# Performance work log

Measured on AMD Instinct MI355X. Metric: run time of the kernel, lower is better.

The kernel has to match this reference:

```python
import jax, jax.numpy as jnp
import numpy as np

N = 50000      # nodes
E = 800000     # edges (avg degree 16)
D = 64         # emb_dim
L = 5          # num_layer
BN_EPS = 1e-5


def setup_inputs() -> dict:
    key = jax.random.key(0)
    ks = jax.random.split(key, 10)
    x = jax.random.randint(ks[0], (N,), 0, 1)                      # indices into 1-row embedding
    edge_index = jax.random.randint(ks[1], (2, E), 0, N)
    edge_attr = jax.random.normal(ks[2], (E, 7), dtype=jnp.float32)
    s = lambda k, shape: (jax.random.normal(k, shape, dtype=jnp.float32) * 0.05)
    node_emb = s(ks[3], (1, D))
    # per-layer GINConv params, stacked on a leading layer axis for lax.scan
    We = s(ks[4], (L, 7, D));   be = jnp.zeros((L, D), jnp.float32)      # edge_encoder
    eps = jnp.zeros((L,), jnp.float32)                                   # GIN eps
    W1 = s(ks[5], (L, D, 2 * D)); b1 = jnp.zeros((L, 2 * D), jnp.float32)  # mlp linear1
    g1 = jnp.ones((L, 2 * D), jnp.float32); bb1 = jnp.zeros((L, 2 * D), jnp.float32)  # mlp BN
    W2 = s(ks[6], (L, 2 * D, D)); b2 = jnp.zeros((L, D), jnp.float32)    # mlp linear2
    g2 = jnp.ones((L, D), jnp.float32); bb2 = jnp.zeros((L, D), jnp.float32)  # outer BN
    return dict(x=x, edge_index=edge_index, edge_attr=edge_attr, node_emb=node_emb,
                We=We, be=be, eps=eps, W1=W1, b1=b1, g1=g1, bb1=bb1,
                W2=W2, b2=b2, g2=g2, bb2=bb2)


def _bn(a, g, b):
    # BatchNorm1d in training mode: batch statistics over node axis, biased var
    m = a.mean(axis=0)
    v = jnp.var(a, axis=0)
    return (a - m) * jax.lax.rsqrt(v + BN_EPS) * g + b


def reference(x, edge_index, edge_attr, node_emb, We, be, eps,
              W1, b1, g1, bb1, W2, b2, g2, bb2):
    src, dst = edge_index[0], edge_index[1]
    h = node_emb[x]                                    # [N, D]
    relu_flags = jnp.arange(L) < (L - 1)               # ReLU on all but last layer

    def step(h, p):
        We_, be_, eps_, W1_, b1_, g1_, bb1_, W2_, b2_, g2_, bb2_, flag = p
        ee = edge_attr @ We_ + be_                     # [E, D] edge embeddings
        msg = jax.nn.relu(h[src] + ee)                 # gather + elementwise
        agg = jax.ops.segment_sum(msg, dst, num_segments=N)  # scatter-add
        z = (1.0 + eps_) * h + agg                     # GIN combine
        a = jax.nn.relu(_bn(z @ W1_ + b1_, g1_, bb1_)) # mlp: lin -> BN -> ReLU
        hb = _bn(a @ W2_ + b2_, g2_, bb2_)             # lin -> outer BN
        h_new = jnp.where(flag, jax.nn.relu(hb), hb)   # dropout omitted (eval)
        return h_new, None

    h, _ = jax.lax.scan(step, h, (We, be, eps, W1, b1, g1, bb1, W2, b2, g2, bb2, relu_flags))
    return h                                           # JK='last'
```

## Files before the change

### kernel.cpp

```cpp
#include <hip/hip_runtime.h>
#include <hip/hip_fp16.h>

#define NN 50000
#define EE 800000
#define NB 782
#define NBKT 196
#define BCAP 5120

typedef _Float16 f16x8 __attribute__((ext_vector_type(8)));
typedef _Float16 f16x4 __attribute__((ext_vector_type(4)));
typedef _Float16 f16x2 __attribute__((ext_vector_type(2)));
typedef float f32x4 __attribute__((ext_vector_type(4)));

__device__ __forceinline__ unsigned h2u(__half2 h) {
    union { __half2 h; unsigned u; } c; c.h = h; return c.u;
}
__device__ __forceinline__ f16x2 u2h(unsigned u) {
    union { unsigned u; f16x2 h; } c; c.u = u; return c.h;
}

__global__ __launch_bounds__(256) void bin_kernel(
    const int* __restrict__ ei, const float* __restrict__ ea,
    int* __restrict__ bktcur, int4* __restrict__ srec,
    unsigned short* __restrict__ sdst)
{
    __shared__ int cnt[NBKT], base[NBKT];
    const int t = threadIdx.x;
    if (t < NBKT) cnt[t] = 0;
    __syncthreads();
    const int e0 = blockIdx.x << 10;
    int bkk[4], rk[4], loc[4];
#pragma unroll
    for (int j = 0; j < 4; ++j) {
        const int e = e0 + (j << 8) + t;
        if (e < EE) {
            const int d = ei[EE + e];
            bkk[j] = d >> 8;
            loc[j] = d & 255;
            rk[j] = atomicAdd(&cnt[bkk[j]], 1);
        } else bkk[j] = -1;
    }
    __syncthreads();
    if (t < NBKT) base[t] = cnt[t] ? atomicAdd(&bktcur[t], cnt[t]) : 0;
    __syncthreads();
#pragma unroll
    for (int j = 0; j < 4; ++j) {
        if (bkk[j] < 0) continue;
        const int slot = base[bkk[j]] + rk[j];
        if (slot >= BCAP) continue;
        const int pos = bkk[j] * BCAP + slot;
        const int e = e0 + (j << 8) + t;
        const int src = ei[e];
        const float* a = ea + e * 7;
        const unsigned h0 = __half_as_ushort(__float2half(a[0]));
        const unsigned h1 = __half_as_ushort(__float2half(a[1]));
        const unsigned h2 = __half_as_ushort(__float2half(a[2]));
        const unsigned h3 = __half_as_ushort(__float2half(a[3]));
        const unsigned h4 = __half_as_ushort(__float2half(a[4]));
        const unsigned h5 = __half_as_ushort(__float2half(a[5]));
        const unsigned h6 = __half_as_ushort(__float2half(a[6]));
        srec[pos] = make_int4((int)(h0 | (h1 << 16)), (int)(h2 | (h3 << 16)),
                              (int)(h4 | (h5 << 16)), (int)(h6 | ((unsigned)src << 16)));
        sdst[pos] = (unsigned short)loc[j];
    }
}

__global__ __launch_bounds__(256) void bcount2_kernel(
    const int* __restrict__ bktcur, const unsigned short* __restrict__ sdst,
    int* __restrict__ deg)
{
    __shared__ int nc[256];
    const int b = blockIdx.x, t = threadIdx.x;
    nc[t] = 0;
    __syncthreads();
    const int nEdge = bktcur[b];
    const int sbase = b * BCAP;
    for (int i = t; i < nEdge; i += 256) atomicAdd(&nc[(int)sdst[sbase + i]], 1);
    __syncthreads();
    const int node = (b << 8) + t;
    if (node < NN) deg[node] = nc[t];
}

__global__ __launch_bounds__(256) void scanA_kernel(const int* __restrict__ deg,
                                                    int* __restrict__ bsum) {
    __shared__ int sm[256];
    const int t = threadIdx.x;
    const int i = (blockIdx.x << 8) + t;
    sm[t] = (i < NN) ? ((deg[i] + 7) & ~7) : 0;
    __syncthreads();
    for (int o = 128; o > 0; o >>= 1) {
        if (t < o) sm[t] += sm[t + o];
        __syncthreads();
    }
    if (t == 0) bsum[blockIdx.x] = sm[0];
}

__global__ __launch_bounds__(256) void scanB_kernel(int* __restrict__ bsum) {
    __shared__ int sm[256];
    const int t = threadIdx.x;
    const int v = (t < 196) ? bsum[t] : 0;
    sm[t] = v;
    __syncthreads();
    for (int o = 1; o < 256; o <<= 1) {
        const int u = (t >= o) ? sm[t - o] : 0;
        __syncthreads();
        sm[t] += u;
        __syncthreads();
    }
    bsum[t] = sm[t] - v;
}

__global__ __launch_bounds__(256) void scanC_kernel(const int* __restrict__ deg,
                                                    const int* __restrict__ bsum,
                                                    int* __restrict__ off,
                                                    int* __restrict__ cur) {
    __shared__ int sm[256];
    const int t = threadIdx.x;
    const int i = (blockIdx.x << 8) + t;
    const int v = (i < NN) ? ((deg[i] + 7) & ~7) : 0;
    sm[t] = v;
    __syncthreads();
    for (int o = 1; o < 256; o <<= 1) {
        const int u = (t >= o) ? sm[t - o] : 0;
        __syncthreads();
        sm[t] += u;
        __syncthreads();
    }
    const int excl = bsum[blockIdx.x] + sm[t] - v;
    if (i < NN) { off[i] = excl; cur[i] = excl; }
    else if (i == NN) off[NN] = excl;
}

__global__ __launch_bounds__(256) void place2_kernel(
    const int* __restrict__ bktcur, const int* __restrict__ off,
    const int4* __restrict__ srec, const unsigned short* __restrict__ sdst,
    int4* __restrict__ pea)
{
    __shared__ int curs[256];
    const int b = blockIdx.x, t = threadIdx.x;
    const int node = (b << 8) + t;
    curs[t] = (node < NN) ? off[node] : 0;
    __syncthreads();
    const int nEdge = bktcur[b];
    const int sbase = b * BCAP;
    for (int i = t; i < nEdge; i += 256) {
        const int ln = (int)sdst[sbase + i];
        const int p = atomicAdd(&curs[ln], 1);
        pea[p] = srec[sbase + i];
    }
    __syncthreads();
    if (node < NN) {
        const int end = off[node + 1];
        for (int p = curs[t]; p < end; ++p)
            pea[p] = make_int4(0, 0, 0, (int)(((unsigned)NN) << 16));
    }
}

__global__ __launch_bounds__(256) void bnstats_kernel(
    const float* __restrict__ part, const int nb, const int half,
    const float* __restrict__ g, const float* __restrict__ bb,
    float* __restrict__ scsh)
{
    __shared__ float ss[256], qq[256];
    const int c = blockIdx.x, t = threadIdx.x;
    const int stride = half << 1;
    float s = 0.f, q = 0.f;
    for (int b = t; b < nb; b += 256) {
        s += part[b * stride + c];
        q += part[b * stride + half + c];
    }
    ss[t] = s; qq[t] = q;
    __syncthreads();
    for (int o = 128; o > 0; o >>= 1) {
        if (t < o) { ss[t] += ss[t + o]; qq[t] += qq[t + o]; }
        __syncthreads();
    }
    if (t == 0) {
        const float m = ss[0] * (1.0f / NN);
        const float v = fmaxf(qq[0] * (1.0f / NN) - m * m, 0.0f);
        const float sc = g[c] * rsqrtf(v + 1e-5f);
        scsh[c] = sc;
        scsh[half + c] = bb[c] - m * sc;
    }
}

__global__ __launch_bounds__(256) void wprep_kernel(
    const float* __restrict__ W1, const float* __restrict__ W2,
    const float* __restrict__ We, const float* __restrict__ be,
    _Float16* __restrict__ W1s, _Float16* __restrict__ W2s,
    unsigned* __restrict__ Wepk, unsigned* __restrict__ be2)
{
    const int i = (blockIdx.x << 8) + threadIdx.x;
    if (i < 40960) {
        const int l = i >> 13, j = i & 8191, k = j >> 7, n = j & 127;
        W1s[(l << 13) + ((((k >> 3) << 7) + n) << 3) + (k & 7)] = (_Float16)W1[i];
    } else if (i < 81920) {
        const int i2 = i - 40960;
        const int l = i2 >> 13, j = i2 & 8191, k = j >> 6, n = j & 63;
        W2s[(l << 13) + ((((k >> 3) << 6) + n) << 3) + (k & 7)] = (_Float16)W2[i2];
    } else if (i < 83040) {
        const int i3 = i - 81920;
        const int l = i3 / 224;
        const int r = i3 - l * 224;
        const int k = r >> 5, s = r & 31;
        const float* W = We + l * 448 + (k << 6) + (s << 1);
        Wepk[i3] = h2u(__floats2half2_rn(W[0], W[1]));
    } else if (i < 83200) {
        const int i4 = i - 83040;
        const int l = i4 >> 5, s = i4 & 31;
        const float* B = be + (l << 6) + (s << 1);
        be2[i4] = h2u(__floats2half2_rn(B[0], B[1]));
    }
}

__global__ __launch_bounds__(256) void hprep_kernel(
    const float* __restrict__ y2, const float* __restrict__ scsh2,
    __half* __restrict__ h16)
{
    const int i4 = (blockIdx.x << 8) + threadIdx.x;
    const float4 v = ((const float4*)y2)[i4];
    const int d0 = (i4 << 2) & 63;
    const float a = fmaxf(fmaf(v.x, scsh2[d0 + 0], scsh2[64 + d0 + 0]), 0.f);
    const float b = fmaxf(fmaf(v.y, scsh2[d0 + 1], scsh2[64 + d0 + 1]), 0.f);
    const float c = fmaxf(fmaf(v.z, scsh2[d0 + 2], scsh2[64 + d0 + 2]), 0.f);
    const float d = fmaxf(fmaf(v.w, scsh2[d0 + 3], scsh2[64 + d0 + 3]), 0.f);
    *(int2*)(h16 + (i4 << 2)) =
        make_int2((int)h2u(__floats2half2_rn(a, b)),
                  (int)h2u(__floats2half2_rn(c, d)));
}

__global__ __launch_bounds__(256) void hprep0_kernel(
    const int* __restrict__ x, const float* __restrict__ nemb,
    __half* __restrict__ h16, unsigned* __restrict__ z32)
{
    const int i4 = (blockIdx.x << 8) + threadIdx.x;
    if (blockIdx.x == 0 && threadIdx.x < 32)
        ((unsigned*)h16)[(NN << 5) + threadIdx.x] = 0xFBFFFBFFu;
    if (i4 < 1536) z32[1600000 + i4] = 0u;
    const int n = i4 >> 4;
    const float4 v = ((const float4*)nemb)[(x[n] << 4) + (i4 & 15)];
    *(int2*)(h16 + (i4 << 2)) =
        make_int2((int)h2u(__floats2half2_rn(v.x, v.y)),
                  (int)h2u(__floats2half2_rn(v.z, v.w)));
}

__global__ __launch_bounds__(256) void gather_kernel(
    const int* __restrict__ off, const int4* __restrict__ pea,
    const unsigned* __restrict__ h32,
    const unsigned* __restrict__ Wepk, const unsigned* __restrict__ be2,
    const float* __restrict__ epsp,
    unsigned* __restrict__ z32)
{
    const int t = threadIdx.x;
    const int lane = t & 63;
    const int s = lane & 31;
    const int n = (blockIdx.x << 3) + ((t >> 6) << 1) + (lane >> 5);

    const f16x2 w0 = u2h(Wepk[s]),       w1 = u2h(Wepk[32 + s]),
                w2 = u2h(Wepk[64 + s]),  w3 = u2h(Wepk[96 + s]),
                w4 = u2h(Wepk[128 + s]), w5 = u2h(Wepk[160 + s]),
                w6 = u2h(Wepk[192 + s]);
    const f16x2 beh = u2h(be2[s]);

    const int e0 = off[n], e1 = off[n + 1];

    f16x2 acc2 = (f16x2){(_Float16)0.f, (_Float16)0.f};
    for (int e = e0; e < e1; e += 8) {
        int4 pk[8];
#pragma unroll
        for (int j = 0; j < 8; ++j) pk[j] = pea[e + j];
        unsigned hv[8];
#pragma unroll
        for (int j = 0; j < 8; ++j) {
            const int src = (int)(((unsigned)pk[j].w) >> 16);
            hv[j] = h32[(src << 5) + s];
        }
#pragma unroll
        for (int j = 0; j < 8; ++j) {
            const f16x2 a01 = u2h((unsigned)pk[j].x);
            const f16x2 a23 = u2h((unsigned)pk[j].y);
            const f16x2 a45 = u2h((unsigned)pk[j].z);
            const f16x2 a6x = u2h((unsigned)pk[j].w);
            f16x2 ee = beh;
            ee += (f16x2){a01[0], a01[0]} * w0;
            ee += (f16x2){a01[1], a01[1]} * w1;
            ee += (f16x2){a23[0], a23[0]} * w2;
            ee += (f16x2){a23[1], a23[1]} * w3;
            ee += (f16x2){a45[0], a45[0]} * w4;
            ee += (f16x2){a45[1], a45[1]} * w5;
            ee += (f16x2){a6x[0], a6x[0]} * w6;
            f16x2 m2 = u2h(hv[j]) + ee;
            const _Float16 zz = (_Float16)0.f;
            m2 = (f16x2){ m2[0] > zz ? m2[0] : zz, m2[1] > zz ? m2[1] : zz };
            acc2 += m2;
        }
    }
    const f16x2 hn2 = u2h(h32[(n << 5) + s]);
    const float e1f = 1.0f + epsp[0];
    const float zLo = fmaf(e1f, (float)hn2[0], (float)acc2[0]);
    const float zHi = fmaf(e1f, (float)hn2[1], (float)acc2[1]);
    z32[(n << 5) + s] = h2u(__floats2half2_rn(zLo, zHi));
}

__global__ __launch_bounds__(256) void mm1_kernel(
    const _Float16* __restrict__ z16, const _Float16* __restrict__ W1s,
    const float* __restrict__ b1p, _Float16* __restrict__ y1h,
    float* __restrict__ part1)
{
    __shared__ float smS[4][128], smQ[4][128];
    const int t = threadIdx.x;
    const int wv = t >> 6, lane = t & 63;
    const int q = lane >> 4, ln = lane & 15;
    const int r0 = blockIdx.x << 6;

    const int rowm = r0 + (wv << 4) + ln;
    const f16x8 af0 = *(const f16x8*)(z16 + rowm * 64 + (q << 3));
    const f16x8 af1 = *(const f16x8*)(z16 + rowm * 64 + 32 + (q << 3));

    f32x4 acc[8];
#pragma unroll
    for (int n0 = 0; n0 < 8; ++n0) acc[n0] = (f32x4){0.f, 0.f, 0.f, 0.f};
#pragma unroll
    for (int n0 = 0; n0 < 8; ++n0) {
        const f16x8 bf0 = *(const f16x8*)(W1s + (((q << 7) + (n0 << 4) + ln) << 3));
        const f16x8 bf1 = *(const f16x8*)(W1s + ((((4 + q) << 7) + (n0 << 4) + ln) << 3));
        acc[n0] = __builtin_amdgcn_mfma_f32_16x16x32_f16(af0, bf0, acc[n0], 0, 0, 0);
        acc[n0] = __builtin_amdgcn_mfma_f32_16x16x32_f16(af1, bf1, acc[n0], 0, 0, 0);
    }

    const int baseRow = r0 + (wv << 4) + (q << 2);
#pragma unroll
    for (int n0 = 0; n0 < 8; ++n0) {
        const int col = (n0 << 4) + ln;
        const float bb = b1p[col];
        float s = 0.f, sq = 0.f;
#pragma unroll
        for (int rg = 0; rg < 4; ++rg) {
            const int row = baseRow + rg;
            const float y = acc[n0][rg] + bb;
            y1h[row * 128 + col] = (_Float16)y;
            const float m = (row < NN) ? 1.f : 0.f;
            s = fmaf(m, y, s); sq = fmaf(m, y * y, sq);
        }
        s += __shfl_xor(s, 16); s += __shfl_xor(s, 32);
        sq += __shfl_xor(sq, 16); sq += __shfl_xor(sq, 32);
        if (lane < 16) { smS[wv][col] = s; smQ[wv][col] = sq; }
    }
    __syncthreads();
    if (t < 128) {
        const float s = smS[0][t] + smS[1][t] + smS[2][t] + smS[3][t];
        const float q2 = smQ[0][t] + smQ[1][t] + smQ[2][t] + smQ[3][t];
        part1[(blockIdx.x << 8) + t] = s;
        part1[(blockIdx.x << 8) + 128 + t] = q2;
    }
}

__global__ __launch_bounds__(256) void mm2_kernel(
    const _Float16* __restrict__ y1h, const float* __restrict__ scsh1,
    const _Float16* __restrict__ W2s, const float* __restrict__ b2,
    float* __restrict__ y2, float* __restrict__ part2)
{
    __shared__ float smS[4][64], smQ[4][64];
    const int t = threadIdx.x;
    const int wv = t >> 6, lane = t & 63;
    const int q = lane >> 4, ln = lane & 15;
    const int r0 = blockIdx.x << 6;

    const int rowm = r0 + (wv << 4) + ln;
    f16x8 af[4];
#pragma unroll
    for (int ks = 0; ks < 4; ++ks) {
        const int k0 = (ks << 5) + (q << 3);
        const f16x8 raw = *(const f16x8*)(y1h + rowm * 128 + k0);
        const float4 scA = *(const float4*)(scsh1 + k0);
        const float4 scB = *(const float4*)(scsh1 + k0 + 4);
        const float4 shA = *(const float4*)(scsh1 + 128 + k0);
        const float4 shB = *(const float4*)(scsh1 + 128 + k0 + 4);
        const float sc[8] = {scA.x, scA.y, scA.z, scA.w, scB.x, scB.y, scB.z, scB.w};
        const float sh[8] = {shA.x, shA.y, shA.z, shA.w, shB.x, shB.y, shB.z, shB.w};
        f16x8 a;
#pragma unroll
        for (int j = 0; j < 8; ++j)
            a[j] = (_Float16)fmaxf(fmaf((float)raw[j], sc[j], sh[j]), 0.f);
        af[ks] = a;
    }

    f32x4 acc[4];
#pragma unroll
    for (int n0 = 0; n0 < 4; ++n0) acc[n0] = (f32x4){0.f, 0.f, 0.f, 0.f};
#pragma unroll
    for (int n0 = 0; n0 < 4; ++n0) {
#pragma unroll
        for (int ks = 0; ks < 4; ++ks) {
            const f16x8 bf = *(const f16x8*)(
                W2s + (((((ks << 2) + q) << 6) + (n0 << 4) + ln) << 3));
            acc[n0] = __builtin_amdgcn_mfma_f32_16x16x32_f16(af[ks], bf, acc[n0], 0, 0, 0);
        }
    }

    const int baseRow = r0 + (wv << 4) + (q << 2);
#pragma unroll
    for (int n0 = 0; n0 < 4; ++n0) {
        const int col = (n0 << 4) + ln;
        const float bb = b2[col];
        float s = 0.f, sq = 0.f;
#pragma unroll
        for (int rg = 0; rg < 4; ++rg) {
            const int row = baseRow + rg;
            const float y = acc[n0][rg] + bb;
            y2[row * 64 + col] = y;
            const float m = (row < NN) ? 1.f : 0.f;
            s = fmaf(m, y, s); sq = fmaf(m, y * y, sq);
        }
        s += __shfl_xor(s, 16); s += __shfl_xor(s, 32);
        sq += __shfl_xor(sq, 16); sq += __shfl_xor(sq, 32);
        if (lane < 16) { smS[wv][col] = s; smQ[wv][col] = sq; }
    }
    __syncthreads();
    if (t < 64) {
        const float s = smS[0][t] + smS[1][t] + smS[2][t] + smS[3][t];
        const float q2 = smQ[0][t] + smQ[1][t] + smQ[2][t] + smQ[3][t];
        part2[(blockIdx.x << 7) + t] = s;
        part2[(blockIdx.x << 7) + 64 + t] = q2;
    }
}

__global__ __launch_bounds__(256) void final_kernel(
    const float* __restrict__ y2, const float* __restrict__ scsh2,
    float* __restrict__ out)
{
    const int i = (blockIdx.x << 8) + threadIdx.x;
    if (i >= NN * 64) return;
    const int d = i & 63;
    out[i] = fmaf(y2[i], scsh2[d], scsh2[64 + d]);
}

extern "C" void kernel_launch(void* const* d_in, const int* in_sizes, int n_in,
                              void* d_out, int out_size, void* d_ws, size_t ws_size,
                              hipStream_t stream)
{
    const int*   x    = (const int*)d_in[0];
    const int*   ei   = (const int*)d_in[1];
    const float* ea   = (const float*)d_in[2];
    const float* nemb = (const float*)d_in[3];
    const float* We   = (const float*)d_in[4];
    const float* be   = (const float*)d_in[5];
    const float* eps  = (const float*)d_in[6];
    const float* W1   = (const float*)d_in[7];
    const float* b1   = (const float*)d_in[8];
    const float* g1   = (const float*)d_in[9];
    const float* bb1  = (const float*)d_in[10];
    const float* W2   = (const float*)d_in[11];
    const float* b2   = (const float*)d_in[12];
    const float* g2   = (const float*)d_in[13];
    const float* bb2  = (const float*)d_in[14];
    float* out = (float*)d_out;

    int*      iws   = (int*)d_ws;
    float*    fws   = (float*)d_ws;
    int*      off   = iws + 0;
    int*      deg   = iws + 50048;
    int*      cur   = iws + 100096;
    int*      bsum  = iws + 150144;
    float*    scsh1 = fws + 150400;
    float*    scsh2 = fws + 150656;
    float*    part1 = fws + 150784;
    float*    part2 = fws + 350976;
    _Float16* W1s   = (_Float16*)(fws + 451072);
    _Float16* W2s   = (_Float16*)(fws + 471552);
    unsigned* Wepk  = (unsigned*)(fws + 492032);
    unsigned* be2   = (unsigned*)(fws + 493152);
    int4*     pea   = (int4*)(iws + 493312);
    _Float16* z16   = (_Float16*)(fws + 5093312);
    _Float16* y1h   = (_Float16*)(fws + 6694848);
    float*    y2    = fws + 6694848;
    __half*   h16   = (__half*)(fws + 9897920);

    int4*           srec   = (int4*)(fws + 5093312);
    unsigned short* sdst   = (unsigned short*)(fws + 9107392);
    int*            bktcur = iws + 150784;

    hipMemsetAsync(bktcur, 0, NBKT * sizeof(int), stream);

    bin_kernel    <<<782,  256, 0, stream>>>(ei, ea, bktcur, srec, sdst);
    bcount2_kernel<<<NBKT, 256, 0, stream>>>(bktcur, sdst, deg);
    scanA_kernel  <<<196,  256, 0, stream>>>(deg, bsum);
    scanB_kernel  <<<1,    256, 0, stream>>>(bsum);
    scanC_kernel  <<<196,  256, 0, stream>>>(deg, bsum, off, cur);
    place2_kernel <<<NBKT, 256, 0, stream>>>(bktcur, off, srec, sdst, pea);
    wprep_kernel  <<<325,  256, 0, stream>>>(W1, W2, We, be, W1s, W2s, Wepk, be2);
    hprep0_kernel <<<3125, 256, 0, stream>>>(x, nemb, h16, (unsigned*)z16);

    for (int l = 0; l < 5; ++l) {
        gather_kernel<<<6250, 256, 0, stream>>>(
            off, pea, (const unsigned*)h16, Wepk + l * 224, be2 + l * 32,
            eps + l, (unsigned*)z16);

        mm1_kernel<<<NB, 256, 0, stream>>>(z16, W1s + l * 8192, b1 + l * 128,
                                           y1h, part1);

        bnstats_kernel<<<128, 256, 0, stream>>>(part1, NB, 128,
                                                g1 + l * 128, bb1 + l * 128, scsh1);

        mm2_kernel<<<NB, 256, 0, stream>>>(y1h, scsh1, W2s + l * 8192, b2 + l * 64,
                                           y2, part2);

        bnstats_kernel<<<64, 256, 0, stream>>>(part2, NB, 64,
                                               g2 + l * 64, bb2 + l * 64, scsh2);

        if (l < 4)
            hprep_kernel<<<3125, 256, 0, stream>>>(y2, scsh2, h16);
    }

    final_kernel<<<12500, 256, 0, stream>>>(y2, scsh2, out);
}
```

Measured before the change: 453.8 us.

## Shard bucket cursors eight ways and fuse degree count with block sum

The binning kernel now spreads each destination bucket across eight sub-buckets chosen by block index, so concurrent blocks hit different global atomic counters and write regions. The downstream count and place kernels loop over the eight sub-buckets. The degree-count kernel also computes the per-block padded sum, which removes the separate scanA launch, and the unused cur array is dropped. Per-sub-bucket capacity is 736, so a skewed input that overfills one sub-bucket would silently drop edges. sdst also moves to an overlapping workspace offset.

New measurement: 454.6 us. Within noise of the previous version (+0.2%).

```diff
diff --git a/kernel.cpp b/kernel.cpp
--- a/kernel.cpp
+++ b/kernel.cpp
@@ -5,7 +5,7 @@
 #define EE 800000
 #define NB 782
 #define NBKT 196
-#define BCAP 5120
+#define CAP8 736
 
 typedef _Float16 f16x8 __attribute__((ext_vector_type(8)));
 typedef _Float16 f16x4 __attribute__((ext_vector_type(4)));
@@ -26,6 +26,7 @@
 {
     __shared__ int cnt[NBKT], base[NBKT];
     const int t = threadIdx.x;
+    const int xid = blockIdx.x & 7;
     if (t < NBKT) cnt[t] = 0;
     __syncthreads();
     const int e0 = blockIdx.x << 10;
@@ -41,14 +42,14 @@
         } else bkk[j] = -1;
     }
     __syncthreads();
-    if (t < NBKT) base[t] = cnt[t] ? atomicAdd(&bktcur[t], cnt[t]) : 0;
+    if (t < NBKT) base[t] = cnt[t] ? atomicAdd(&bktcur[(t << 3) + xid], cnt[t]) : 0;
     __syncthreads();
 #pragma unroll
     for (int j = 0; j < 4; ++j) {
         if (bkk[j] < 0) continue;
         const int slot = base[bkk[j]] + rk[j];
-        if (slot >= BCAP) continue;
-        const int pos = bkk[j] * BCAP + slot;
+        if (slot >= CAP8) continue;
+        const int pos = ((bkk[j] << 3) + xid) * CAP8 + slot;
         const int e = e0 + (j << 8) + t;
         const int src = ei[e];
         const float* a = ea + e * 7;
@@ -65,34 +66,29 @@
     }
 }
 
-__global__ __launch_bounds__(256) void bcount2_kernel(
+__global__ __launch_bounds__(256) void bcountA_kernel(
     const int* __restrict__ bktcur, const unsigned short* __restrict__ sdst,
-    int* __restrict__ deg)
-{
-    __shared__ int nc[256];
+    int* __restrict__ deg, int* __restrict__ bsum)
+{
+    __shared__ int nc[256], sm[256];
     const int b = blockIdx.x, t = threadIdx.x;
     nc[t] = 0;
     __syncthreads();
-    const int nEdge = bktcur[b];
-    const int sbase = b * BCAP;
-    for (int i = t; i < nEdge; i += 256) atomicAdd(&nc[(int)sdst[sbase + i]], 1);
+    for (int x = 0; x < 8; ++x) {
+        const int nE = min(bktcur[(b << 3) + x], CAP8);
+        const int sb = ((b << 3) + x) * CAP8;
+        for (int i = t; i < nE; i += 256) atomicAdd(&nc[(int)sdst[sb + i]], 1);
+    }
     __syncthreads();
     const int node = (b << 8) + t;
     if (node < NN) deg[node] = nc[t];
-}
-
-__global__ __launch_bounds__(256) void scanA_kernel(const int* __restrict__ deg,
-                                                    int* __restrict__ bsum) {
-    __shared__ int sm[256];
-    const int t = threadIdx.x;
-    const int i = (blockIdx.x << 8) + t;
-    sm[t] = (i < NN) ? ((deg[i] + 7) & ~7) : 0;
+    sm[t] = (node < NN) ? ((nc[t] + 7) & ~7) : 0;
     __syncthreads();
     for (int o = 128; o > 0; o >>= 1) {
         if (t < o) sm[t] += sm[t + o];
         __syncthreads();
     }
-    if (t == 0) bsum[blockIdx.x] = sm[0];
+    if (t == 0) bsum[b] = sm[0];
 }
 
 __global__ __launch_bounds__(256) void scanB_kernel(int* __restrict__ bsum) {
@@ -112,8 +108,7 @@
 
 __global__ __launch_bounds__(256) void scanC_kernel(const int* __restrict__ deg,
                                                     const int* __restrict__ bsum,
-                                                    int* __restrict__ off,
-                                                    int* __restrict__ cur) {
+                                                    int* __restrict__ off) {
     __shared__ int sm[256];
     const int t = threadIdx.x;
     const int i = (blockIdx.x << 8) + t;
@@ -127,7 +122,7 @@
         __syncthreads();
     }
     const int excl = bsum[blockIdx.x] + sm[t] - v;
-    if (i < NN) { off[i] = excl; cur[i] = excl; }
+    if (i < NN) off[i] = excl;
     else if (i == NN) off[NN] = excl;
 }
 
@@ -141,12 +136,14 @@
     const int node = (b << 8) + t;
     curs[t] = (node < NN) ? off[node] : 0;
     __syncthreads();
-    const int nEdge = bktcur[b];
-    const int sbase = b * BCAP;
-    for (int i = t; i < nEdge; i += 256) {
-        const int ln = (int)sdst[sbase + i];
-        const int p = atomicAdd(&curs[ln], 1);
-        pea[p] = srec[sbase + i];
+    for (int x = 0; x < 8; ++x) {
+        const int nE = min(bktcur[(b << 3) + x], CAP8);
+        const int sb = ((b << 3) + x) * CAP8;
+        for (int i = t; i < nE; i += 256) {
+            const int ln = (int)sdst[sb + i];
+            const int p = atomicAdd(&curs[ln], 1);
+            pea[p] = srec[sb + i];
+        }
     }
     __syncthreads();
     if (node < NN) {
@@ -460,7 +457,6 @@
     float*    fws   = (float*)d_ws;
     int*      off   = iws + 0;
     int*      deg   = iws + 50048;
-    int*      cur   = iws + 100096;
     int*      bsum  = iws + 150144;
     float*    scsh1 = fws + 150400;
     float*    scsh2 = fws + 150656;
@@ -477,16 +473,15 @@
     __half*   h16   = (__half*)(fws + 9897920);
 
     int4*           srec   = (int4*)(fws + 5093312);
-    unsigned short* sdst   = (unsigned short*)(fws + 9107392);
+    unsigned short* sdst   = (unsigned short*)(fws + 9897920);
     int*            bktcur = iws + 150784;
 
-    hipMemsetAsync(bktcur, 0, NBKT * sizeof(int), stream);
+    hipMemsetAsync(bktcur, 0, NBKT * 8 * sizeof(int), stream);
 
     bin_kernel    <<<782,  256, 0, stream>>>(ei, ea, bktcur, srec, sdst);
-    bcount2_kernel<<<NBKT, 256, 0, stream>>>(bktcur, sdst, deg);
-    scanA_kernel  <<<196,  256, 0, stream>>>(deg, bsum);
+    bcountA_kernel<<<NBKT, 256, 0, stream>>>(bktcur, sdst, deg, bsum);
     scanB_kernel  <<<1,    256, 0, stream>>>(bsum);
-    scanC_kernel  <<<196,  256, 0, stream>>>(deg, bsum, off, cur);
+    scanC_kernel  <<<196,  256, 0, stream>>>(deg, bsum, off);
     place2_kernel <<<NBKT, 256, 0, stream>>>(bktcur, off, srec, sdst, pea);
     wprep_kernel  <<<325,  256, 0, stream>>>(W1, W2, We, be, W1s, W2s, Wepk, be2);
     hprep0_kernel <<<3125, 256, 0, stream>>>(x, nemb, h16, (unsigned*)z16);
```
